# Kernel tuning notes

Hardware: AMD Instinct MI355X
Metric: run time of the kernel (lower is better)

Reference implementation:

```python
import jax, jax.numpy as jnp
import numpy as np

D_MODEL = 1024
D_STATE = 16
D_CONV = 4
EXPAND = 2
INNER = EXPAND * D_MODEL          # 2048
DT_RANK = (D_MODEL + 15) // 16     # 64 ('auto' heuristic)
BATCH = 1
SEQLEN = 2048
DT_MIN, DT_MAX, DT_FLOOR = 1e-3, 1e-1, 1e-4


def setup_inputs() -> dict:
    key = jax.random.key(0)
    ks = jax.random.split(key, 8)
    hidden_states = jax.random.normal(ks[0], (BATCH, SEQLEN, D_MODEL), jnp.float32)
    W_in = jax.random.normal(ks[1], (2 * INNER, D_MODEL), jnp.float32) * (D_MODEL ** -0.5)
    conv_w = jax.random.normal(ks[2], (INNER, D_CONV), jnp.float32) * 0.02
    conv_b = jnp.zeros((INNER,), jnp.float32)
    W_x = jax.random.normal(ks[3], (DT_RANK + 2 * D_STATE, INNER), jnp.float32) * (INNER ** -0.5)
    dt_init_std = DT_RANK ** -0.5
    W_dt = jax.random.uniform(ks[4], (INNER, DT_RANK), jnp.float32, -dt_init_std, dt_init_std)
    # dt_bias = inverse-softplus of dt sampled log-uniform in [dt_min, dt_max]
    dt = jnp.exp(jax.random.uniform(ks[5], (INNER,), jnp.float32)
                 * (np.log(DT_MAX) - np.log(DT_MIN)) + np.log(DT_MIN))
    dt = jnp.clip(dt, DT_FLOOR)
    dt_bias = dt + jnp.log(-jnp.expm1(-dt))
    A_log = jax.random.normal(ks[6], (INNER, D_STATE), jnp.float32) * 0.5
    D_skip = jnp.ones((INNER,), jnp.float32)
    W_out = jax.random.normal(ks[7], (D_MODEL, INNER), jnp.float32) * (INNER ** -0.5)
    return dict(hidden_states=hidden_states, W_in=W_in, conv_w=conv_w, conv_b=conv_b,
                W_x=W_x, W_dt=W_dt, dt_bias=dt_bias, A_log=A_log, D_skip=D_skip, W_out=W_out)


def _silu(x):
    return x * jax.nn.sigmoid(x)


def reference(hidden_states, W_in, conv_w, conv_b, W_x, W_dt, dt_bias, A_log, D_skip, W_out):
    # in_proj: (B, L, d_model) -> (B, L, 2*inner), split into x-branch and gate
    xz = hidden_states @ W_in.T
    proj, gate = jnp.split(xz, 2, axis=-1)

    # depthwise causal conv along L with silu activation
    xc = proj.transpose(0, 2, 1)                       # (B, inner, L)
    kernel = conv_w[:, None, :]                        # (inner, 1, d_conv)
    conv = jax.lax.conv_general_dilated(
        xc, kernel, window_strides=(1,), padding=[(D_CONV - 1, 0)],
        dimension_numbers=('NCH', 'OIH', 'NCH'), feature_group_count=INNER)
    conv = _silu(conv + conv_b[None, :, None])         # (B, inner, L)
    u = conv.transpose(0, 2, 1)                        # (B, L, inner)

    # x_proj -> low-rank dt, B, C per-token
    projt = u @ W_x.T                                  # (B, L, dt_rank + 2*N)
    dt_lr, Bp, Cp = jnp.split(projt, [DT_RANK, DT_RANK + D_STATE], axis=-1)
    delta = jax.nn.softplus(dt_lr @ W_dt.T + dt_bias)  # (B, L, inner)

    # selective scan: h_t = exp(delta*A) h_{t-1} + delta*B_t*u_t
    A = -jnp.exp(A_log)                                # (inner, N)
    dA = jnp.exp(jnp.einsum('bld,dn->lbdn', delta, A))            # (L,B,inner,N)
    dBu = jnp.einsum('bld,bln,bld->lbdn', delta, Bp, u)           # (L,B,inner,N)

    def step(h, inp):
        dA_t, dBu_t = inp
        h = dA_t * h + dBu_t
        return h, h

    h0 = jnp.zeros((hidden_states.shape[0], INNER, D_STATE), u.dtype)
    _, hs = jax.lax.scan(step, h0, (dA, dBu))          # (L,B,inner,N)

    y = jnp.einsum('lbdn,bln->bld', hs, Cp)            # (B, L, inner)
    y = y + D_skip * u                                 # D skip connection
    y = y * _silu(gate)                                # gated output
    return y @ W_out.T                                 # (B, L, d_model)
```

## Files before the change

kernel.cpp:

```cpp
#include <hip/hip_runtime.h>
#include <hip/hip_bf16.h>

#define SEQLEN 2048
#define DMODEL 1024
#define INNER  2048
#define DSTATE 16
#define DTRANK 64
#define NPROJ  96
#define NPAD   128
#define CHUNK  16
#define NCH    128
#define KSPLIT 16

typedef __attribute__((ext_vector_type(8))) short bf16x8;
typedef __attribute__((ext_vector_type(4))) float f32x4;

__device__ __forceinline__ float softplusf(float x) {
    return (x > 20.f) ? x : log1pf(__expf(x));
}
__device__ __forceinline__ unsigned short f2bf(float x) {
    unsigned u = __float_as_uint(x);
    return (unsigned short)((u + 0x7FFF + ((u >> 16) & 1)) >> 16);
}
__device__ __forceinline__ float bf2f(unsigned short x) {
    return __uint_as_float((unsigned)x << 16);
}
__device__ __forceinline__ void gload_lds16(const void* g, void* l) {
    __builtin_amdgcn_global_load_lds(
        (__attribute__((address_space(1))) const unsigned int*)g,
        (__attribute__((address_space(3))) unsigned int*)l,
        16, 0, 0);
}
__device__ __forceinline__ void cvt8(const float* __restrict__ in,
                                     unsigned short* __restrict__ out, int i) {
    float4 a = ((const float4*)in)[2 * i];
    float4 b = ((const float4*)in)[2 * i + 1];
    uint4 v;
    v.x = f2bf(a.x) | ((unsigned)f2bf(a.y) << 16);
    v.y = f2bf(a.z) | ((unsigned)f2bf(a.w) << 16);
    v.z = f2bf(b.x) | ((unsigned)f2bf(b.y) << 16);
    v.w = f2bf(b.z) | ((unsigned)f2bf(b.w) << 16);
    ((uint4*)out)[i] = v;
}

__global__ __launch_bounds__(256)
void cvt_all(const float* __restrict__ hidden, const float* __restrict__ W_in,
             const float* __restrict__ W_out, const float* __restrict__ W_dt,
             const float* __restrict__ W_x,
             unsigned short* __restrict__ hid_b, unsigned short* __restrict__ Win_b,
             unsigned short* __restrict__ Wout_b, unsigned short* __restrict__ Wdt_b,
             unsigned short* __restrict__ Wx_b)
{
    int i = blockIdx.x * 256 + threadIdx.x;
    if (i < 262144) { cvt8(hidden, hid_b, i); return; }
    i -= 262144;
    if (i < 524288) { cvt8(W_in, Win_b, i); return; }
    i -= 524288;
    if (i < 262144) { cvt8(W_out, Wout_b, i); return; }
    i -= 262144;
    if (i < 16384)  { cvt8(W_dt, Wdt_b, i); return; }
    i -= 16384;
    if (i < 32768) {
        int row = i >> 8;
        if (row < NPROJ) cvt8(W_x, Wx_b, i);
        else ((uint4*)Wx_b)[i] = make_uint4(0, 0, 0, 0);
    }
}

template<int BM, int BN, int EPI>
__global__ __launch_bounds__(256)
void gemm_bf16(const unsigned short* __restrict__ A, const int lda,
               const unsigned short* __restrict__ B, const int ldb,
               void* __restrict__ Cv, const int ldc, const long long zCstride,
               const int K, const int kspan, const float* __restrict__ bias)
{
    constexpr int FM = BM / 32;
    constexpr int FN = BN / 32;
    __shared__ alignas(16) short As[BM * 64];
    __shared__ alignas(16) short Bs[BN * 64];

    const int tid  = threadIdx.x;
    const int wave = tid >> 6;
    const int lane = tid & 63;

    int bid = blockIdx.y * gridDim.x + blockIdx.x;
    const int q = (gridDim.x * gridDim.y) >> 3;
    bid = (bid & 7) * q + (bid >> 3);
    const int bx = bid % gridDim.x;
    const int by = bid / gridDim.x;

    const long long row0 = (long long)by * BM;
    const long long col0 = (long long)bx * BN;
    const int wm = (wave >> 1) * (BM / 2);
    const int wn = (wave & 1) * (BN / 2);
    const int kstart = blockIdx.z * kspan;
    const int kend   = min(K, kstart + kspan);

    f32x4 acc[FM][FN] = {};

    const int srow   = tid >> 3;
    const int schunk = (tid & 7) ^ (srow & 7);
    const unsigned short* gA = A + (row0 + srow) * lda + schunk * 8;
    const unsigned short* gB = B + (col0 + srow) * ldb + schunk * 8;
    short* lA = &As[srow * 64 + (tid & 7) * 8];
    short* lB = &Bs[srow * 64 + (tid & 7) * 8];

    const int fr = lane & 15;
    const int hi = lane >> 4;
    const int rb = fr & 7;

    for (int kt = kstart; kt < kend; kt += 64) {
#pragma unroll
        for (int r = 0; r < BM; r += 32)
            gload_lds16(gA + (long long)r * lda + kt, lA + r * 64);
#pragma unroll
        for (int r = 0; r < BN; r += 32)
            gload_lds16(gB + (long long)r * ldb + kt, lB + r * 64);
        __syncthreads();

#pragma unroll
        for (int half = 0; half < 2; ++half) {
            const int kc = (((half << 2) + hi) ^ rb) * 8;
            bf16x8 af[FM], bfr[FN];
#pragma unroll
            for (int mi = 0; mi < FM; ++mi)
                af[mi] = *(const bf16x8*)&As[(wm + mi * 16 + fr) * 64 + kc];
#pragma unroll
            for (int ni = 0; ni < FN; ++ni)
                bfr[ni] = *(const bf16x8*)&Bs[(wn + ni * 16 + fr) * 64 + kc];
#pragma unroll
            for (int mi = 0; mi < FM; ++mi)
#pragma unroll
                for (int ni = 0; ni < FN; ++ni)
                    acc[mi][ni] = __builtin_amdgcn_mfma_f32_16x16x32_bf16(
                        af[mi], bfr[ni], acc[mi][ni], 0, 0, 0);
        }
        __syncthreads();
    }

    const int cr = hi * 4;
#pragma unroll
    for (int mi = 0; mi < FM; ++mi)
#pragma unroll
        for (int ni = 0; ni < FN; ++ni) {
            long long rbase = row0 + wm + mi * 16 + cr;
            long long col   = col0 + wn + ni * 16 + fr;
#pragma unroll
            for (int r = 0; r < 4; ++r) {
                long long idx = (rbase + r) * ldc + col;
                if (EPI == 0) {
                    ((float*)Cv)[(long long)blockIdx.z * zCstride + idx] = acc[mi][ni][r];
                } else if (EPI == 1) {
                    ((unsigned short*)Cv)[idx] = f2bf(acc[mi][ni][r]);
                } else {
                    ((unsigned short*)Cv)[idx] = f2bf(softplusf(acc[mi][ni][r] + bias[col]));
                }
            }
        }
}

__global__ __launch_bounds__(256)
void xproj_fused(const unsigned short* __restrict__ xz_b,
                 const float* __restrict__ cw, const float* __restrict__ cb,
                 const unsigned short* __restrict__ Wx_b,
                 unsigned short* __restrict__ u_b, float* __restrict__ Cv)
{
    __shared__ alignas(16) short As[128 * 64];
    __shared__ alignas(16) short Bs[128 * 64];

    const int tid  = threadIdx.x;
    const int wave = tid >> 6;
    const int lane = tid & 63;

    int bid = blockIdx.y;
    bid = (bid & 7) * 2 + (bid >> 3);
    const long long row0 = (long long)bid * 128;

    const int wm = (wave >> 1) * 64;
    const int wn = (wave & 1) * 64;
    const int kstart = blockIdx.z * (INNER / KSPLIT);

    f32x4 acc[2][2] = {};

    const int srow   = tid >> 3;
    const int gchunk = (tid & 7) ^ (srow & 7);
    short* lA = &As[srow * 64 + (tid & 7) * 8];
    short* lB = &Bs[srow * 64 + (tid & 7) * 8];
    const unsigned short* gB = Wx_b + srow * INNER + gchunk * 8;

    const int fr = lane & 15;
    const int hi = lane >> 4;
    const int rb = fr & 7;

    for (int kt = kstart; kt < kstart + 128; kt += 64) {
        const int d = kt + gchunk * 8;
        float4 wv[8];
#pragma unroll
        for (int k = 0; k < 8; ++k) wv[k] = ((const float4*)cw)[d + k];
        float bias8[8];
        {
            float4 c0 = ((const float4*)cb)[d >> 2];
            float4 c1 = ((const float4*)cb)[(d >> 2) + 1];
            bias8[0] = c0.x; bias8[1] = c0.y; bias8[2] = c0.z; bias8[3] = c0.w;
            bias8[4] = c1.x; bias8[5] = c1.y; bias8[6] = c1.z; bias8[7] = c1.w;
        }
#pragma unroll
        for (int r = 0; r < 128; r += 32) {
            const long long l = row0 + srow + r;
            float a[8];
#pragma unroll
            for (int k = 0; k < 8; ++k) a[k] = bias8[k];
#pragma unroll
            for (int j = 0; j < 4; ++j) {
                long long ls = l - 3 + j;
                if (ls >= 0) {
                    bf16x8 x = *(const bf16x8*)&xz_b[ls * 4096 + d];
#pragma unroll
                    for (int k = 0; k < 8; ++k)
                        a[k] = fmaf(((const float*)&wv[k])[j],
                                    bf2f((unsigned short)x[k]), a[k]);
                }
            }
            float s8[8];
#pragma unroll
            for (int k = 0; k < 8; ++k) s8[k] = a[k] / (1.f + __expf(-a[k]));
            uint4 p;
            p.x = f2bf(s8[0]) | ((unsigned)f2bf(s8[1]) << 16);
            p.y = f2bf(s8[2]) | ((unsigned)f2bf(s8[3]) << 16);
            p.z = f2bf(s8[4]) | ((unsigned)f2bf(s8[5]) << 16);
            p.w = f2bf(s8[6]) | ((unsigned)f2bf(s8[7]) << 16);
            *(uint4*)(lA + r * 64) = p;
            *(uint4*)&u_b[l * INNER + d] = p;
        }
#pragma unroll
        for (int r = 0; r < 128; r += 32)
            gload_lds16(gB + (long long)r * INNER + kt, lB + r * 64);
        __syncthreads();

#pragma unroll
        for (int half = 0; half < 2; ++half) {
            const int kc = (((half << 2) + hi) ^ rb) * 8;
            bf16x8 af[2], bfr[2];
#pragma unroll
            for (int mi = 0; mi < 2; ++mi)
                af[mi] = *(const bf16x8*)&As[(wm + mi * 16 + fr) * 64 + kc];
#pragma unroll
            for (int ni = 0; ni < 2; ++ni)
                bfr[ni] = *(const bf16x8*)&Bs[(wn + ni * 16 + fr) * 64 + kc];
#pragma unroll
            for (int mi = 0; mi < 2; ++mi)
#pragma unroll
                for (int ni = 0; ni < 2; ++ni)
                    acc[mi][ni] = __builtin_amdgcn_mfma_f32_16x16x32_bf16(
                        af[mi], bfr[ni], acc[mi][ni], 0, 0, 0);
        }
        __syncthreads();
    }

    const int cr = hi * 4;
#pragma unroll
    for (int mi = 0; mi < 2; ++mi)
#pragma unroll
        for (int ni = 0; ni < 2; ++ni) {
            long long rbase = row0 + wm + mi * 16 + cr;
            long long col   = wn + ni * 16 + fr;
#pragma unroll
            for (int r = 0; r < 4; ++r)
                Cv[(long long)blockIdx.z * (SEQLEN * NPAD) +
                   (rbase + r) * NPAD + col] = acc[mi][ni][r];
        }
}

__global__ __launch_bounds__(256)
void reduce_out(const float* __restrict__ part, float* __restrict__ out)
{
    int i = blockIdx.x * 256 + threadIdx.x;
    float4 a = ((const float4*)part)[i];
    float4 b = ((const float4*)part)[i + SEQLEN * DMODEL / 4];
    a.x += b.x; a.y += b.y; a.z += b.z; a.w += b.w;
    ((float4*)out)[i] = a;
}

__global__ __launch_bounds__(256)
void reduce_part(const float* __restrict__ part, float* __restrict__ projt,
                 unsigned short* __restrict__ projt_b)
{
    int i = blockIdx.x * 256 + threadIdx.x;
    float s = 0.f;
#pragma unroll
    for (int z = 0; z < KSPLIT; ++z) s += part[(long long)z * SEQLEN * NPAD + i];
    projt[i] = s;
    projt_b[i] = f2bf(s);
}

__global__ __launch_bounds__(256)
void scan_phase1(const unsigned short* __restrict__ delta_bf,
                 const unsigned short* __restrict__ u_b,
                 const float* __restrict__ projt, const float* __restrict__ A_log,
                 unsigned short* __restrict__ Slocb, float* __restrict__ sumd)
{
    __shared__ float Bsh[CHUNK][16];
    const int d  = blockIdx.x * 256 + threadIdx.x;
    const int c  = blockIdx.y;
    const int l0 = c * CHUNK;
    for (int i = threadIdx.x; i < CHUNK * 16; i += 256) {
        int l = i >> 4, j = i & 15;
        Bsh[l][j] = projt[(l0 + l) * NPAD + DTRANK + j];
    }
    __syncthreads();

    float A2[DSTATE];
#pragma unroll
    for (int n = 0; n < DSTATE; ++n)
        A2[n] = -__expf(A_log[d * DSTATE + n]) * 1.4426950408889634f;

    float dl[CHUNK], du[CHUNK];
#pragma unroll
    for (int t = 0; t < CHUNK; ++t) {
        int l = l0 + t;
        float dv = bf2f(delta_bf[l * INNER + d]);
        dl[t] = dv;
        du[t] = dv * bf2f(u_b[l * INNER + d]);
    }

    float h[DSTATE];
#pragma unroll
    for (int n = 0; n < DSTATE; ++n) h[n] = 0.f;
    float sd = 0.f;

#pragma unroll
    for (int t = 0; t < CHUNK; ++t) {
        sd += dl[t];
#pragma unroll
        for (int n = 0; n < DSTATE; ++n) {
            float dA = exp2f(dl[t] * A2[n]);
            h[n] = fmaf(dA, h[n], du[t] * Bsh[t][n]);
        }
    }
    uint4 p0, p1;
    p0.x = f2bf(h[0])  | ((unsigned)f2bf(h[1])  << 16);
    p0.y = f2bf(h[2])  | ((unsigned)f2bf(h[3])  << 16);
    p0.z = f2bf(h[4])  | ((unsigned)f2bf(h[5])  << 16);
    p0.w = f2bf(h[6])  | ((unsigned)f2bf(h[7])  << 16);
    p1.x = f2bf(h[8])  | ((unsigned)f2bf(h[9])  << 16);
    p1.y = f2bf(h[10]) | ((unsigned)f2bf(h[11]) << 16);
    p1.z = f2bf(h[12]) | ((unsigned)f2bf(h[13]) << 16);
    p1.w = f2bf(h[14]) | ((unsigned)f2bf(h[15]) << 16);
    uint4* dst = (uint4*)&Slocb[(long long)(c * INNER + d) * DSTATE];
    dst[0] = p0; dst[1] = p1;
    sumd[c * INNER + d] = sd;
}

__global__ __launch_bounds__(256)
void scan_phase2(unsigned short* __restrict__ S, const float* __restrict__ sumd,
                 const float* __restrict__ A_log)
{
    int i = blockIdx.x * 256 + threadIdx.x;
    int d = i >> 4;
    float A2 = -__expf(A_log[i]) * 1.4426950408889634f;
    float H = 0.f;
#pragma unroll
    for (int c = 0; c < NCH; ++c) {
        float s = bf2f(S[c * (INNER * DSTATE) + i]);
        float P = exp2f(A2 * sumd[c * INNER + d]);
        S[c * (INNER * DSTATE) + i] = f2bf(H);
        H = fmaf(P, H, s);
    }
}

__global__ __launch_bounds__(256)
void scan_phase3(const unsigned short* __restrict__ delta_bf,
                 const unsigned short* __restrict__ u_b,
                 const float* __restrict__ projt, const float* __restrict__ A_log,
                 const unsigned short* __restrict__ Hinit,
                 const unsigned short* __restrict__ xz_b,
                 const float* __restrict__ D_skip, unsigned short* __restrict__ ybf)
{
    __shared__ float BC[CHUNK][32];
    const int d  = blockIdx.x * 256 + threadIdx.x;
    const int c  = blockIdx.y;
    const int l0 = c * CHUNK;
    for (int i = threadIdx.x; i < CHUNK * 32; i += 256) {
        int l = i >> 5, j = i & 31;
        BC[l][j] = projt[(l0 + l) * NPAD + DTRANK + j];
    }
    __syncthreads();

    float A2[DSTATE];
#pragma unroll
    for (int n = 0; n < DSTATE; ++n)
        A2[n] = -__expf(A_log[d * DSTATE + n]) * 1.4426950408889634f;

    float dl[CHUNK], uv[CHUNK];
#pragma unroll
    for (int t = 0; t < CHUNK; ++t) {
        int l = l0 + t;
        dl[t] = bf2f(delta_bf[l * INNER + d]);
        uv[t] = bf2f(u_b[l * INNER + d]);
    }

    float h[DSTATE];
    {
        const uint4* hp = (const uint4*)&Hinit[(long long)(c * INNER + d) * DSTATE];
        uint4 p0 = hp[0], p1 = hp[1];
        h[0]  = bf2f((unsigned short)(p0.x & 0xffff)); h[1]  = bf2f((unsigned short)(p0.x >> 16));
        h[2]  = bf2f((unsigned short)(p0.y & 0xffff)); h[3]  = bf2f((unsigned short)(p0.y >> 16));
        h[4]  = bf2f((unsigned short)(p0.z & 0xffff)); h[5]  = bf2f((unsigned short)(p0.z >> 16));
        h[6]  = bf2f((unsigned short)(p0.w & 0xffff)); h[7]  = bf2f((unsigned short)(p0.w >> 16));
        h[8]  = bf2f((unsigned short)(p1.x & 0xffff)); h[9]  = bf2f((unsigned short)(p1.x >> 16));
        h[10] = bf2f((unsigned short)(p1.y & 0xffff)); h[11] = bf2f((unsigned short)(p1.y >> 16));
        h[12] = bf2f((unsigned short)(p1.z & 0xffff)); h[13] = bf2f((unsigned short)(p1.z >> 16));
        h[14] = bf2f((unsigned short)(p1.w & 0xffff)); h[15] = bf2f((unsigned short)(p1.w >> 16));
    }
    const float Dd = D_skip[d];

#pragma unroll
    for (int t = 0; t < CHUNK; ++t) {
        int l = l0 + t;
        float du = dl[t] * uv[t];
        float y = 0.f;
#pragma unroll
        for (int n = 0; n < DSTATE; ++n) {
            float dA = exp2f(dl[t] * A2[n]);
            h[n] = fmaf(dA, h[n], du * BC[t][n]);
            y = fmaf(h[n], BC[t][16 + n], y);
        }
        float yv = fmaf(Dd, uv[t], y);
        float g = bf2f(xz_b[(long long)l * 4096 + 2048 + d]);
        float sg = g / (1.f + __expf(-g));
        ybf[l * INNER + d] = f2bf(yv * sg);
    }
}

extern "C" void kernel_launch(void* const* d_in, const int* in_sizes, int n_in,
                              void* d_out, int out_size, void* d_ws, size_t ws_size,
                              hipStream_t stream)
{
    const float* hidden  = (const float*)d_in[0];
    const float* W_in    = (const float*)d_in[1];
    const float* conv_w  = (const float*)d_in[2];
    const float* conv_b  = (const float*)d_in[3];
    const float* W_x     = (const float*)d_in[4];
    const float* W_dt    = (const float*)d_in[5];
    const float* dt_bias = (const float*)d_in[6];
    const float* A_log   = (const float*)d_in[7];
    const float* D_skip  = (const float*)d_in[8];
    const float* W_out   = (const float*)d_in[9];
    float* out = (float*)d_out;

    char* base = (char*)d_ws;
    unsigned short* xz_b    = (unsigned short*)(base + 0);
    unsigned short* hid_b   = (unsigned short*)(base + 16777216);
    unsigned short* Win_b   = (unsigned short*)(base + 20971520);
    unsigned short* u_b     = (unsigned short*)(base + 16777216);
    float*          part16  = (float*)(base + 25165824);
    unsigned short* Slocb   = (unsigned short*)(base + 25165824);
    float*          opart   = (float*)(base + 25165824);
    unsigned short* dlt_b   = (unsigned short*)(base + 41943040);
    unsigned short* y_b     = (unsigned short*)(base + 50331648);
    float*          projt   = (float*)(base + 58720256);
    unsigned short* projt_b = (unsigned short*)(base + 59768832);
    unsigned short* Wout_b  = (unsigned short*)(base + 60293120);
    unsigned short* Wx_b    = (unsigned short*)(base + 64487424);
    unsigned short* Wdt_b   = (unsigned short*)(base + 65011712);
    float*          sumd    = (float*)(base + 65273856);

    cvt_all<<<4289, 256, 0, stream>>>(hidden, W_in, W_out, W_dt, W_x,
                                      hid_b, Win_b, Wout_b, Wdt_b, Wx_b);

    gemm_bf16<128, 128, 1><<<dim3(32, 16, 1), 256, 0, stream>>>(
        hid_b, DMODEL, Win_b, DMODEL, xz_b, 4096, 0, DMODEL, DMODEL, nullptr);

    xproj_fused<<<dim3(1, 16, KSPLIT), 256, 0, stream>>>(
        xz_b, conv_w, conv_b, Wx_b, u_b, part16);
    reduce_part<<<SEQLEN * NPAD / 256, 256, 0, stream>>>(part16, projt, projt_b);

    gemm_bf16<128, 64, 2><<<dim3(32, 16, 1), 256, 0, stream>>>(
        projt_b, NPAD, Wdt_b, DTRANK, dlt_b, INNER, 0, DTRANK, DTRANK, dt_bias);

    scan_phase1<<<dim3(INNER / 256, NCH), 256, 0, stream>>>(dlt_b, u_b, projt, A_log, Slocb, sumd);
    scan_phase2<<<(INNER * DSTATE) / 256, 256, 0, stream>>>(Slocb, sumd, A_log);
    scan_phase3<<<dim3(INNER / 256, NCH), 256, 0, stream>>>(dlt_b, u_b, projt, A_log,
                                                            Slocb, xz_b, D_skip, y_b);

    gemm_bf16<128, 64, 0><<<dim3(16, 16, 2), 256, 0, stream>>>(
        y_b, INNER, Wout_b, INNER, opart, DMODEL, (long long)SEQLEN * DMODEL,
        INNER, INNER / 2, nullptr);
    reduce_out<<<SEQLEN * DMODEL / 1024, 256, 0, stream>>>(opart, out);
}
```

Baseline: 161.1 us.

## Fuse dt projection and softplus into scan phase 1 and phase 3 prologues

Removes the separate delta GEMM kernel and its bf16 delta buffer. Each scan block now computes its 16x256 delta tile with MFMA from projt_b and W_dt, applies bias and softplus, and keeps the tile in LDS. This saves one launch and the write and two reads of a 2048x2048 bf16 tensor. In exchange the small GEMM and the softplus are computed twice (in phase 1 and phase 3), and each scan block does extra work before its sync.

```diff
diff --git a/kernel.cpp b/kernel.cpp
--- a/kernel.cpp
+++ b/kernel.cpp
@@ -72,7 +72,7 @@
 void gemm_bf16(const unsigned short* __restrict__ A, const int lda,
                const unsigned short* __restrict__ B, const int ldb,
                void* __restrict__ Cv, const int ldc, const long long zCstride,
-               const int K, const int kspan, const float* __restrict__ bias)
+               const int K, const int kspan)
 {
     constexpr int FM = BM / 32;
     constexpr int FN = BN / 32;
@@ -150,10 +150,8 @@
                 long long idx = (rbase + r) * ldc + col;
                 if (EPI == 0) {
                     ((float*)Cv)[(long long)blockIdx.z * zCstride + idx] = acc[mi][ni][r];
-                } else if (EPI == 1) {
+                } else {
                     ((unsigned short*)Cv)[idx] = f2bf(acc[mi][ni][r]);
-                } else {
-                    ((unsigned short*)Cv)[idx] = f2bf(softplusf(acc[mi][ni][r] + bias[col]));
                 }
             }
         }
@@ -293,20 +291,61 @@
     projt_b[i] = f2bf(s);
 }
 
-__global__ __launch_bounds__(256)
-void scan_phase1(const unsigned short* __restrict__ delta_bf,
+__device__ __forceinline__ void delta_prologue(
+    const unsigned short* __restrict__ projt_b,
+    const unsigned short* __restrict__ Wdt_b,
+    const float* __restrict__ dt_bias,
+    int l0, int d0, int tid, unsigned short (*dlds)[256])
+{
+    const int wv   = tid >> 6;
+    const int lane = tid & 63;
+    const int fr   = lane & 15;
+    const int hi   = lane >> 4;
+
+    bf16x8 a[2];
+#pragma unroll
+    for (int ks = 0; ks < 2; ++ks)
+        a[ks] = *(const bf16x8*)&projt_b[(l0 + fr) * NPAD + ks * 32 + hi * 8];
+
+    f32x4 acc[4] = {};
+#pragma unroll
+    for (int ni = 0; ni < 4; ++ni) {
+        const int d = d0 + wv * 64 + ni * 16 + fr;
+#pragma unroll
+        for (int ks = 0; ks < 2; ++ks) {
+            bf16x8 b = *(const bf16x8*)&Wdt_b[d * DTRANK + ks * 32 + hi * 8];
+            acc[ni] = __builtin_amdgcn_mfma_f32_16x16x32_bf16(a[ks], b, acc[ni], 0, 0, 0);
+        }
+    }
+#pragma unroll
+    for (int ni = 0; ni < 4; ++ni) {
+        const int dcol = wv * 64 + ni * 16 + fr;
+        const float bias = dt_bias[d0 + dcol];
+#pragma unroll
+        for (int r = 0; r < 4; ++r)
+            dlds[hi * 4 + r][dcol] = f2bf(softplusf(acc[ni][r] + bias));
+    }
+}
+
+__global__ __launch_bounds__(256)
+void scan_phase1(const unsigned short* __restrict__ projt_b,
+                 const unsigned short* __restrict__ Wdt_b,
+                 const float* __restrict__ dt_bias,
                  const unsigned short* __restrict__ u_b,
                  const float* __restrict__ projt, const float* __restrict__ A_log,
                  unsigned short* __restrict__ Slocb, float* __restrict__ sumd)
 {
     __shared__ float Bsh[CHUNK][16];
-    const int d  = blockIdx.x * 256 + threadIdx.x;
-    const int c  = blockIdx.y;
-    const int l0 = c * CHUNK;
-    for (int i = threadIdx.x; i < CHUNK * 16; i += 256) {
+    __shared__ unsigned short dlds[CHUNK][256];
+    const int tid = threadIdx.x;
+    const int d   = blockIdx.x * 256 + tid;
+    const int c   = blockIdx.y;
+    const int l0  = c * CHUNK;
+    for (int i = tid; i < CHUNK * 16; i += 256) {
         int l = i >> 4, j = i & 15;
         Bsh[l][j] = projt[(l0 + l) * NPAD + DTRANK + j];
     }
+    delta_prologue(projt_b, Wdt_b, dt_bias, l0, blockIdx.x * 256, tid, dlds);
     __syncthreads();
 
     float A2[DSTATE];
@@ -318,7 +357,7 @@
 #pragma unroll
     for (int t = 0; t < CHUNK; ++t) {
         int l = l0 + t;
-        float dv = bf2f(delta_bf[l * INNER + d]);
+        float dv = bf2f(dlds[t][tid]);
         dl[t] = dv;
         du[t] = dv * bf2f(u_b[l * INNER + d]);
     }
@@ -369,7 +408,9 @@
 }
 
 __global__ __launch_bounds__(256)
-void scan_phase3(const unsigned short* __restrict__ delta_bf,
+void scan_phase3(const unsigned short* __restrict__ projt_b,
+                 const unsigned short* __restrict__ Wdt_b,
+                 const float* __restrict__ dt_bias,
                  const unsigned short* __restrict__ u_b,
                  const float* __restrict__ projt, const float* __restrict__ A_log,
                  const unsigned short* __restrict__ Hinit,
@@ -377,13 +418,16 @@
                  const float* __restrict__ D_skip, unsigned short* __restrict__ ybf)
 {
     __shared__ float BC[CHUNK][32];
-    const int d  = blockIdx.x * 256 + threadIdx.x;
-    const int c  = blockIdx.y;
-    const int l0 = c * CHUNK;
-    for (int i = threadIdx.x; i < CHUNK * 32; i += 256) {
+    __shared__ unsigned short dlds[CHUNK][256];
+    const int tid = threadIdx.x;
+    const int d   = blockIdx.x * 256 + tid;
+    const int c   = blockIdx.y;
+    const int l0  = c * CHUNK;
+    for (int i = tid; i < CHUNK * 32; i += 256) {
         int l = i >> 5, j = i & 31;
         BC[l][j] = projt[(l0 + l) * NPAD + DTRANK + j];
     }
+    delta_prologue(projt_b, Wdt_b, dt_bias, l0, blockIdx.x * 256, tid, dlds);
     __syncthreads();
 
     float A2[DSTATE];
@@ -395,7 +439,7 @@
 #pragma unroll
     for (int t = 0; t < CHUNK; ++t) {
         int l = l0 + t;
-        dl[t] = bf2f(delta_bf[l * INNER + d]);
+        dl[t] = bf2f(dlds[t][tid]);
         uv[t] = bf2f(u_b[l * INNER + d]);
     }
 
@@ -456,7 +500,6 @@
     float*          part16  = (float*)(base + 25165824);
     unsigned short* Slocb   = (unsigned short*)(base + 25165824);
     float*          opart   = (float*)(base + 25165824);
-    unsigned short* dlt_b   = (unsigned short*)(base + 41943040);
     unsigned short* y_b     = (unsigned short*)(base + 50331648);
     float*          projt   = (float*)(base + 58720256);
     unsigned short* projt_b = (unsigned short*)(base + 59768832);
@@ -469,22 +512,20 @@
                                       hid_b, Win_b, Wout_b, Wdt_b, Wx_b);
 
     gemm_bf16<128, 128, 1><<<dim3(32, 16, 1), 256, 0, stream>>>(
-        hid_b, DMODEL, Win_b, DMODEL, xz_b, 4096, 0, DMODEL, DMODEL, nullptr);
+        hid_b, DMODEL, Win_b, DMODEL, xz_b, 4096, 0, DMODEL, DMODEL);
 
     xproj_fused<<<dim3(1, 16, KSPLIT), 256, 0, stream>>>(
         xz_b, conv_w, conv_b, Wx_b, u_b, part16);
     reduce_part<<<SEQLEN * NPAD / 256, 256, 0, stream>>>(part16, projt, projt_b);
 
-    gemm_bf16<128, 64, 2><<<dim3(32, 16, 1), 256, 0, stream>>>(
-        projt_b, NPAD, Wdt_b, DTRANK, dlt_b, INNER, 0, DTRANK, DTRANK, dt_bias);
-
-    scan_phase1<<<dim3(INNER / 256, NCH), 256, 0, stream>>>(dlt_b, u_b, projt, A_log, Slocb, sumd);
+    scan_phase1<<<dim3(INNER / 256, NCH), 256, 0, stream>>>(
+        projt_b, Wdt_b, dt_bias, u_b, projt, A_log, Slocb, sumd);
     scan_phase2<<<(INNER * DSTATE) / 256, 256, 0, stream>>>(Slocb, sumd, A_log);
-    scan_phase3<<<dim3(INNER / 256, NCH), 256, 0, stream>>>(dlt_b, u_b, projt, A_log,
-                                                            Slocb, xz_b, D_skip, y_b);
+    scan_phase3<<<dim3(INNER / 256, NCH), 256, 0, stream>>>(
+        projt_b, Wdt_b, dt_bias, u_b, projt, A_log, Slocb, xz_b, D_skip, y_b);
 
     gemm_bf16<128, 64, 0><<<dim3(16, 16, 2), 256, 0, stream>>>(
         y_b, INNER, Wout_b, INNER, opart, DMODEL, (long long)SEQLEN * DMODEL,
-        INNER, INNER / 2, nullptr);
+        INNER, INNER / 2);
     reduce_out<<<SEQLEN * DMODEL / 1024, 256, 0, stream>>>(opart, out);
 }
```

New measurement: 178.0 us. +10.5%, slower.

## Fuse split-K reduction with dt projection and softplus; shrink scan_phase2 blocks

Applied to the files above, without the earlier changes.

Merges the split-K partial-sum reduction of x_proj with the low-rank dt projection GEMM and softplus epilogue into one kernel. Each block reduces 16 rows, stages the dt_lr slice in LDS as bf16, and runs MFMA against W_dt, writing delta directly. This removes a kernel launch and the projt_b round-trip. The dt GEMM now runs on only 128 blocks, each looping over all 2048 inner columns. scan_phase2 also moves to 64-thread blocks so more blocks spread across CUs.

```diff
diff --git a/kernel.cpp b/kernel.cpp
--- a/kernel.cpp
+++ b/kernel.cpp
@@ -72,7 +72,7 @@
 void gemm_bf16(const unsigned short* __restrict__ A, const int lda,
                const unsigned short* __restrict__ B, const int ldb,
                void* __restrict__ Cv, const int ldc, const long long zCstride,
-               const int K, const int kspan, const float* __restrict__ bias)
+               const int K, const int kspan)
 {
     constexpr int FM = BM / 32;
     constexpr int FN = BN / 32;
@@ -150,10 +150,8 @@
                 long long idx = (rbase + r) * ldc + col;
                 if (EPI == 0) {
                     ((float*)Cv)[(long long)blockIdx.z * zCstride + idx] = acc[mi][ni][r];
-                } else if (EPI == 1) {
+                } else {
                     ((unsigned short*)Cv)[idx] = f2bf(acc[mi][ni][r]);
-                } else {
-                    ((unsigned short*)Cv)[idx] = f2bf(softplusf(acc[mi][ni][r] + bias[col]));
                 }
             }
         }
@@ -282,15 +280,68 @@
 }
 
 __global__ __launch_bounds__(256)
-void reduce_part(const float* __restrict__ part, float* __restrict__ projt,
-                 unsigned short* __restrict__ projt_b)
-{
-    int i = blockIdx.x * 256 + threadIdx.x;
-    float s = 0.f;
-#pragma unroll
-    for (int z = 0; z < KSPLIT; ++z) s += part[(long long)z * SEQLEN * NPAD + i];
-    projt[i] = s;
-    projt_b[i] = f2bf(s);
+void reduce_delta(const float* __restrict__ part,
+                  const unsigned short* __restrict__ Wdt_b,
+                  const float* __restrict__ dt_bias,
+                  float* __restrict__ projt, unsigned short* __restrict__ dlt_b)
+{
+    __shared__ unsigned short albs[16 * 64];
+    const int tid = threadIdx.x;
+    const int l0  = blockIdx.x * 16;
+
+    const int rrow = tid >> 4;
+    const int rcol = (tid & 15) * 8;
+    const long long ibase = (long long)(l0 + rrow) * NPAD + rcol;
+    float4 s0 = make_float4(0.f, 0.f, 0.f, 0.f);
+    float4 s1 = make_float4(0.f, 0.f, 0.f, 0.f);
+#pragma unroll
+    for (int z = 0; z < KSPLIT; ++z) {
+        const float* p = part + (long long)z * SEQLEN * NPAD + ibase;
+        float4 a = ((const float4*)p)[0];
+        float4 b = ((const float4*)p)[1];
+        s0.x += a.x; s0.y += a.y; s0.z += a.z; s0.w += a.w;
+        s1.x += b.x; s1.y += b.y; s1.z += b.z; s1.w += b.w;
+    }
+    ((float4*)&projt[ibase])[0] = s0;
+    ((float4*)&projt[ibase])[1] = s1;
+    if (rcol < 64) {
+        uint4 p;
+        p.x = f2bf(s0.x) | ((unsigned)f2bf(s0.y) << 16);
+        p.y = f2bf(s0.z) | ((unsigned)f2bf(s0.w) << 16);
+        p.z = f2bf(s1.x) | ((unsigned)f2bf(s1.y) << 16);
+        p.w = f2bf(s1.z) | ((unsigned)f2bf(s1.w) << 16);
+        *(uint4*)&albs[rrow * 64 + rcol] = p;
+    }
+    __syncthreads();
+
+    const int wv   = tid >> 6;
+    const int lane = tid & 63;
+    const int fr   = lane & 15;
+    const int hi   = lane >> 4;
+
+    bf16x8 a0 = *(const bf16x8*)&albs[fr * 64 + hi * 8];
+    bf16x8 a1 = *(const bf16x8*)&albs[fr * 64 + 32 + hi * 8];
+
+    for (int d0 = 0; d0 < INNER; d0 += 256) {
+        f32x4 acc[4] = {};
+#pragma unroll
+        for (int ni = 0; ni < 4; ++ni) {
+            const int d = d0 + wv * 64 + ni * 16 + fr;
+            bf16x8 b0 = *(const bf16x8*)&Wdt_b[d * DTRANK + hi * 8];
+            acc[ni] = __builtin_amdgcn_mfma_f32_16x16x32_bf16(a0, b0, acc[ni], 0, 0, 0);
+            bf16x8 b1 = *(const bf16x8*)&Wdt_b[d * DTRANK + 32 + hi * 8];
+            acc[ni] = __builtin_amdgcn_mfma_f32_16x16x32_bf16(a1, b1, acc[ni], 0, 0, 0);
+        }
+#pragma unroll
+        for (int ni = 0; ni < 4; ++ni) {
+            const int dcol = d0 + wv * 64 + ni * 16 + fr;
+            const float bias = dt_bias[dcol];
+#pragma unroll
+            for (int r = 0; r < 4; ++r)
+                dlt_b[(long long)(l0 + hi * 4 + r) * INNER + dcol] =
+                    f2bf(softplusf(acc[ni][r] + bias));
+        }
+    }
 }
 
 __global__ __launch_bounds__(256)
@@ -351,11 +402,11 @@
     sumd[c * INNER + d] = sd;
 }
 
-__global__ __launch_bounds__(256)
+__global__ __launch_bounds__(64)
 void scan_phase2(unsigned short* __restrict__ S, const float* __restrict__ sumd,
                  const float* __restrict__ A_log)
 {
-    int i = blockIdx.x * 256 + threadIdx.x;
+    int i = blockIdx.x * 64 + threadIdx.x;
     int d = i >> 4;
     float A2 = -__expf(A_log[i]) * 1.4426950408889634f;
     float H = 0.f;
@@ -459,7 +510,6 @@
     unsigned short* dlt_b   = (unsigned short*)(base + 41943040);
     unsigned short* y_b     = (unsigned short*)(base + 50331648);
     float*          projt   = (float*)(base + 58720256);
-    unsigned short* projt_b = (unsigned short*)(base + 59768832);
     unsigned short* Wout_b  = (unsigned short*)(base + 60293120);
     unsigned short* Wx_b    = (unsigned short*)(base + 64487424);
     unsigned short* Wdt_b   = (unsigned short*)(base + 65011712);
@@ -469,22 +519,21 @@
                                       hid_b, Win_b, Wout_b, Wdt_b, Wx_b);
 
     gemm_bf16<128, 128, 1><<<dim3(32, 16, 1), 256, 0, stream>>>(
-        hid_b, DMODEL, Win_b, DMODEL, xz_b, 4096, 0, DMODEL, DMODEL, nullptr);
+        hid_b, DMODEL, Win_b, DMODEL, xz_b, 4096, 0, DMODEL, DMODEL);
 
     xproj_fused<<<dim3(1, 16, KSPLIT), 256, 0, stream>>>(
         xz_b, conv_w, conv_b, Wx_b, u_b, part16);
-    reduce_part<<<SEQLEN * NPAD / 256, 256, 0, stream>>>(part16, projt, projt_b);
-
-    gemm_bf16<128, 64, 2><<<dim3(32, 16, 1), 256, 0, stream>>>(
-        projt_b, NPAD, Wdt_b, DTRANK, dlt_b, INNER, 0, DTRANK, DTRANK, dt_bias);
-
-    scan_phase1<<<dim3(INNER / 256, NCH), 256, 0, stream>>>(dlt_b, u_b, projt, A_log, Slocb, sumd);
-    scan_phase2<<<(INNER * DSTATE) / 256, 256, 0, stream>>>(Slocb, sumd, A_log);
-    scan_phase3<<<dim3(INNER / 256, NCH), 256, 0, stream>>>(dlt_b, u_b, projt, A_log,
-                                                            Slocb, xz_b, D_skip, y_b);
+
+    reduce_delta<<<NCH, 256, 0, stream>>>(part16, Wdt_b, dt_bias, projt, dlt_b);
+
+    scan_phase1<<<dim3(INNER / 256, NCH), 256, 0, stream>>>(
+        dlt_b, u_b, projt, A_log, Slocb, sumd);
+    scan_phase2<<<(INNER * DSTATE) / 64, 64, 0, stream>>>(Slocb, sumd, A_log);
+    scan_phase3<<<dim3(INNER / 256, NCH), 256, 0, stream>>>(
+        dlt_b, u_b, projt, A_log, Slocb, xz_b, D_skip, y_b);
 
     gemm_bf16<128, 64, 0><<<dim3(16, 16, 2), 256, 0, stream>>>(
         y_b, INNER, Wout_b, INNER, opart, DMODEL, (long long)SEQLEN * DMODEL,
-        INNER, INNER / 2, nullptr);
+        INNER, INNER / 2);
     reduce_out<<<SEQLEN * DMODEL / 1024, 256, 0, stream>>>(opart, out);
 }
```

Measured after the change: 193.2 us. 1.2x slower.
